# Kernel tuning notes

Measured on AMD Instinct MI355X. Metric: run time of the kernel, lower is better.

## Reference

```python
import jax, jax.numpy as jnp
import numpy as np

EPS = 1e-12  # torch F.normalize clamps the norm at 1e-12

def _l2norm(v, axis):
    n = jnp.sqrt(jnp.sum(v * v, axis=axis, keepdims=True))
    return v / jnp.maximum(n, EPS)

def setup_inputs() -> dict:
    key = jax.random.key(0)
    k1, k2, k3, k4 = jax.random.split(key, 4)
    N, C, H, W, K = 64, 64, 64, 64, 128
    alpha = 1.0
    x = jax.random.normal(k1, (N, C, H, W), dtype=jnp.float32)
    centroids = jax.random.uniform(k2, (K, C), dtype=jnp.float32)
    # conv is initialized from centroids (2*alpha*c, -alpha*||c||) but is an
    # independent parameter after init; keep the init relationship for realism.
    conv_w = 2.0 * alpha * centroids
    conv_b = -alpha * jnp.sqrt(jnp.sum(centroids * centroids, axis=1))
    return {"x": x, "centroids": centroids, "conv_w": conv_w, "conv_b": conv_b}

def reference(x, centroids, conv_w, conv_b):
    N, C, H, W = x.shape
    K = centroids.shape[0]
    # L2-normalize descriptors along channel dim
    xn = _l2norm(x, axis=1)                                   # [N,C,H,W]
    # 1x1 conv == per-pixel linear map C->K
    logits = jnp.einsum('nchw,kc->nkhw', xn, conv_w) + conv_b[None, :, None, None]
    sa = jax.nn.softmax(logits.reshape(N, K, H * W), axis=1)  # [N,K,HW]
    xf = xn.reshape(N, C, H * W)                              # [N,C,HW]
    # vlad[n,k,c] = sum_l sa[n,k,l] * (xf[n,c,l] - centroids[k,c])
    #            = (sa @ xf^T)[n,k,c] - sum_l sa[n,k,l] * centroids[k,c]
    vlad = jnp.einsum('nkl,ncl->nkc', sa, xf) - sa.sum(axis=-1)[:, :, None] * centroids[None]
    vlad = _l2norm(vlad, axis=2)            # intra-normalization per cluster
    vlad = vlad.reshape(N, K * C)
    vlad = _l2norm(vlad, axis=1)            # global L2 normalization
    return vlad
```

## Files before the change

### kernel.cpp

```cpp
#include <hip/hip_runtime.h>
#include <math.h>

#define NIMG   64
#define CDIM   64
#define HWPX   4096
#define KCL    128
#define TL     32
#define SHIFT  10.0f
#define RSQRT128 0.08838834764831845f

#define XP_S 72
#define XC_S 40
#define PH_S 40

typedef __attribute__((ext_vector_type(8))) short short8;
typedef __attribute__((ext_vector_type(4))) float f32x4;

#define MFMA(a, b, c) __builtin_amdgcn_mfma_f32_16x16x32_bf16((a), (b), (c), 0, 0, 0)

#define PERM_HI16 0x07060302u

template <int NP>
__global__ __launch_bounds__(256, 2)
void netvlad_main(const float* __restrict__ x,
                  const float* __restrict__ conv_w,
                  const float* __restrict__ conv_b,
                  float* __restrict__ vout,
                  float* __restrict__ asout,
                  int use_atomic)
{
    constexpr int PIXPART = HWPX / NP;
    constexpr int NCHUNK  = PIXPART / TL;

    __shared__ __align__(16) short xp_hi[TL * XP_S], xp_lo[TL * XP_S];
    __shared__ __align__(16) short xc[CDIM * XC_S];
    __shared__ __align__(16) short ph[KCL * PH_S];
    __shared__ float redA[4 * 33];
    __shared__ float sumP[4 * TL];

    const int t   = threadIdx.x;
    const int w   = t >> 6;
    const int l   = t & 63;
    const int l15 = l & 15, l4 = l >> 4;
    const int n    = blockIdx.x / NP;
    const int part = blockIdx.x - n * NP;
    const int p_s  = t & 31;
    const int sg   = t >> 5;

    short8 wh[2][2], wl[2][2];
    #pragma unroll
    for (int kt = 0; kt < 2; ++kt) {
        const int krow = (2 * w + kt) * 16 + l15;
        #pragma unroll
        for (int ks = 0; ks < 2; ++ks) {
            const float4* wp = (const float4*)(conv_w + krow * CDIM + ks * 32 + l4 * 8);
            float4 wa = wp[0], wb = wp[1];
            float wv[8] = {wa.x, wa.y, wa.z, wa.w, wb.x, wb.y, wb.z, wb.w};
            #pragma unroll
            for (int j = 0; j < 8; ++j) {
                unsigned u = __builtin_bit_cast(unsigned, wv[j]);
                wh[kt][ks][j] = (short)(u >> 16);
                float hf = __builtin_bit_cast(float, u & 0xffff0000u);
                wl[kt][ks][j] = (short)(__builtin_bit_cast(unsigned, wv[j] - hf) >> 16);
            }
        }
    }
    float cbr[2][4];
    #pragma unroll
    for (int kt = 0; kt < 2; ++kt)
        #pragma unroll
        for (int i = 0; i < 4; ++i)
            cbr[kt][i] = conv_b[(2 * w + kt) * 16 + l4 * 4 + i] - SHIFT;

    f32x4 acc2[2][4];
    #pragma unroll
    for (int a = 0; a < 2; ++a)
        #pragma unroll
        for (int b = 0; b < 4; ++b) acc2[a][b] = (f32x4)0.0f;
    float asr[2][4];
    #pragma unroll
    for (int a = 0; a < 2; ++a)
        #pragma unroll
        for (int i = 0; i < 4; ++i) asr[a][i] = 0.f;

    const float* xbase = x + (size_t)n * CDIM * HWPX + part * PIXPART;

    float xv[8];
    #pragma unroll
    for (int j = 0; j < 8; ++j)
        xv[j] = xbase[(sg * 8 + j) * HWPX + p_s];

    for (int ch = 0; ch < NCHUNK; ++ch) {
        float ssq = 0.f;
        #pragma unroll
        for (int j = 0; j < 8; ++j) ssq += xv[j] * xv[j];
        ssq += __shfl_xor(ssq, 32);
        if (l < 32) redA[w * 33 + p_s] = ssq;

        unsigned uh[4], ul[4];
        #pragma unroll
        for (int jp = 0; jp < 4; ++jp) {
            const unsigned u0 = __builtin_bit_cast(unsigned, xv[2 * jp]);
            const unsigned u1 = __builtin_bit_cast(unsigned, xv[2 * jp + 1]);
            uh[jp] = __builtin_amdgcn_perm(u1, u0, PERM_HI16);
            const float h0 = __builtin_bit_cast(float, u0 & 0xffff0000u);
            const float h1 = __builtin_bit_cast(float, u1 & 0xffff0000u);
            const unsigned lo0 = __builtin_bit_cast(unsigned, xv[2 * jp] - h0);
            const unsigned lo1 = __builtin_bit_cast(unsigned, xv[2 * jp + 1] - h1);
            ul[jp] = __builtin_amdgcn_perm(lo1, lo0, PERM_HI16);
        }
        *(uint4*)&xp_hi[p_s * XP_S + sg * 8] = make_uint4(uh[0], uh[1], uh[2], uh[3]);
        *(uint4*)&xp_lo[p_s * XP_S + sg * 8] = make_uint4(ul[0], ul[1], ul[2], ul[3]);

        #pragma unroll
        for (int jp = 0; jp < 4; ++jp) {
            unsigned pk;
            asm("v_cvt_pk_bf16_f32 %0, %1, %2"
                : "=v"(pk) : "v"(xv[2 * jp]), "v"(xv[2 * jp + 1]));
            xc[(sg * 8 + 2 * jp)     * XC_S + p_s] = (short)pk;
            xc[(sg * 8 + 2 * jp + 1) * XC_S + p_s] = (short)(pk >> 16);
        }
        __syncthreads();

        if (ch + 1 < NCHUNK) {
            #pragma unroll
            for (int j = 0; j < 8; ++j)
                xv[j] = xbase[(sg * 8 + j) * HWPX + (ch + 1) * TL + p_s];
        }

        f32x4 a1[2][2];
        #pragma unroll
        for (int a = 0; a < 2; ++a)
            #pragma unroll
            for (int b = 0; b < 2; ++b) a1[a][b] = (f32x4)0.0f;
        #pragma unroll
        for (int ks = 0; ks < 2; ++ks) {
            #pragma unroll
            for (int pt = 0; pt < 2; ++pt) {
                short8 bh = *(short8*)&xp_hi[(pt * 16 + l15) * XP_S + ks * 32 + l4 * 8];
                short8 bl = *(short8*)&xp_lo[(pt * 16 + l15) * XP_S + ks * 32 + l4 * 8];
                #pragma unroll
                for (int kt = 0; kt < 2; ++kt) {
                    a1[kt][pt] = MFMA(wh[kt][ks], bh, a1[kt][pt]);
                    a1[kt][pt] = MFMA(wh[kt][ks], bl, a1[kt][pt]);
                    a1[kt][pt] = MFMA(wl[kt][ks], bh, a1[kt][pt]);
                }
            }
        }

        float rn[2];
        #pragma unroll
        for (int pt = 0; pt < 2; ++pt) {
            const int col = pt * 16 + l15;
            float s0 = redA[col] + redA[33 + col];
            float s1 = redA[2 * 33 + col] + redA[3 * 33 + col];
            rn[pt] = 1.0f / fmaxf(sqrtf(s0 + s1), 1e-12f);
        }

        float e[2][2][4], sp[2] = {0.f, 0.f};
        #pragma unroll
        for (int kt = 0; kt < 2; ++kt)
            #pragma unroll
            for (int pt = 0; pt < 2; ++pt)
                #pragma unroll
                for (int i = 0; i < 4; ++i) {
                    float ev = __expf(fmaf(a1[kt][pt][i], rn[pt], cbr[kt][i]));
                    e[kt][pt][i] = ev;
                    sp[pt] += ev;
                }
        #pragma unroll
        for (int pt = 0; pt < 2; ++pt) {
            sp[pt] += __shfl_xor(sp[pt], 16);
            sp[pt] += __shfl_xor(sp[pt], 32);
        }
        if (l4 == 0) {
            sumP[w * TL + l15]      = sp[0];
            sumP[w * TL + 16 + l15] = sp[1];
        }
        __syncthreads();

        float rden[2], rdn2[2];
        #pragma unroll
        for (int pt = 0; pt < 2; ++pt) {
            const int col = pt * 16 + l15;
            float den = sumP[col] + sumP[TL + col] + sumP[2 * TL + col] + sumP[3 * TL + col];
            rden[pt] = 1.0f / den;
            rdn2[pt] = rden[pt] * rn[pt];
        }

        #pragma unroll
        for (int kt = 0; kt < 2; ++kt)
            #pragma unroll
            for (int i = 0; i < 4; ++i) {
                const int row = (2 * w + kt) * 16 + l4 * 4 + i;
                const float e0 = e[kt][0][i], e1 = e[kt][1][i];
                asr[kt][i] = fmaf(e0, rden[0], asr[kt][i]);
                asr[kt][i] = fmaf(e1, rden[1], asr[kt][i]);
                const float p0 = e0 * rdn2[0], p1 = e1 * rdn2[1];
                unsigned pk;
                asm("v_cvt_pk_bf16_f32 %0, %1, %2" : "=v"(pk) : "v"(p0), "v"(p1));
                ph[row * PH_S + l15]      = (short)pk;
                ph[row * PH_S + 16 + l15] = (short)(pk >> 16);
            }

        {
            short8 xh2[4];
            #pragma unroll
            for (int ct = 0; ct < 4; ++ct)
                xh2[ct] = *(short8*)&xc[(ct * 16 + l15) * XC_S + l4 * 8];
            #pragma unroll
            for (int kt = 0; kt < 2; ++kt) {
                short8 ah = *(short8*)&ph[((2 * w + kt) * 16 + l15) * PH_S + l4 * 8];
                #pragma unroll
                for (int ct = 0; ct < 4; ++ct)
                    acc2[kt][ct] = MFMA(ah, xh2[ct], acc2[kt][ct]);
            }
        }
        __syncthreads();
    }

    float* vg = use_atomic ? vout + (size_t)n * KCL * CDIM
                           : vout + (size_t)blockIdx.x * KCL * CDIM;
    #pragma unroll
    for (int kt = 0; kt < 2; ++kt)
        #pragma unroll
        for (int ct = 0; ct < 4; ++ct)
            #pragma unroll
            for (int i = 0; i < 4; ++i) {
                const int row = (2 * w + kt) * 16 + l4 * 4 + i;
                const int col = ct * 16 + l15;
                if (use_atomic) atomicAdd(&vg[row * CDIM + col], acc2[kt][ct][i]);
                else            vg[row * CDIM + col] = acc2[kt][ct][i];
            }

    #pragma unroll
    for (int kt = 0; kt < 2; ++kt)
        #pragma unroll
        for (int i = 0; i < 4; ++i) {
            float v = asr[kt][i];
            v += __shfl_xor(v, 1); v += __shfl_xor(v, 2);
            v += __shfl_xor(v, 4); v += __shfl_xor(v, 8);
            if (l15 == 0) {
                const int row = (2 * w + kt) * 16 + l4 * 4 + i;
                if (use_atomic) atomicAdd(&asout[n * KCL + row], v);
                else            asout[blockIdx.x * KCL + row] = v;
            }
        }
}

__global__ __launch_bounds__(256)
void netvlad_finalize(const float* __restrict__ vpart,
                      const float* __restrict__ aspart,
                      const float* __restrict__ cent,
                      float* __restrict__ out,
                      int nparts)
{
    const int t = threadIdx.x;
    const int n  = blockIdx.x >> 3;
    const int kg = blockIdx.x & 7;
    const int k  = kg * 16 + (t >> 4);
    const int c0 = (t & 15) * 4;

    float vsum[4] = {0.f, 0.f, 0.f, 0.f};
    float av = 0.f;
    for (int pt = 0; pt < nparts; ++pt) {
        const float* vg = vpart + (((size_t)n * nparts + pt) * KCL + k) * CDIM + c0;
        float4 a = *(const float4*)vg;
        vsum[0] += a.x; vsum[1] += a.y; vsum[2] += a.z; vsum[3] += a.w;
        av += aspart[(n * nparts + pt) * KCL + k];
    }

    float4 cq = *(const float4*)(cent + k * CDIM + c0);
    float cc[4] = {cq.x, cq.y, cq.z, cq.w};
    float ss = 0.f;
    #pragma unroll
    for (int j = 0; j < 4; ++j) {
        vsum[j] -= av * cc[j];
        ss += vsum[j] * vsum[j];
    }
    ss += __shfl_xor(ss, 1); ss += __shfl_xor(ss, 2);
    ss += __shfl_xor(ss, 4); ss += __shfl_xor(ss, 8);
    const float s = (1.0f / fmaxf(sqrtf(ss), 1e-12f)) * RSQRT128;

    float4 o;
    o.x = vsum[0] * s; o.y = vsum[1] * s; o.z = vsum[2] * s; o.w = vsum[3] * s;
    *(float4*)(out + (size_t)n * KCL * CDIM + k * CDIM + c0) = o;
}

extern "C" void kernel_launch(void* const* d_in, const int* in_sizes, int n_in,
                              void* d_out, int out_size, void* d_ws, size_t ws_size,
                              hipStream_t stream) {
    const float* x     = (const float*)d_in[0];
    const float* cent  = (const float*)d_in[1];
    const float* convw = (const float*)d_in[2];
    const float* convb = (const float*)d_in[3];
    float* out = (float*)d_out;

    const size_t need8 = (size_t)NIMG * 8 * (KCL * CDIM + KCL) * sizeof(float);

    if (ws_size >= need8) {
        float* vws  = (float*)d_ws;
        float* asws = vws + (size_t)NIMG * 8 * KCL * CDIM;
        netvlad_main<8><<<dim3(NIMG * 8), dim3(256), 0, stream>>>(
            x, convw, convb, vws, asws, 0);
        netvlad_finalize<<<dim3(NIMG * 8), dim3(256), 0, stream>>>(
            vws, asws, cent, out, 8);
    } else {
        float* vws  = (float*)d_ws;
        float* asws = vws + (size_t)NIMG * KCL * CDIM;
        const size_t zb = (size_t)NIMG * (KCL * CDIM + KCL) * sizeof(float);
        hipMemsetAsync(d_ws, 0, zb, stream);
        netvlad_main<8><<<dim3(NIMG * 8), dim3(256), 0, stream>>>(
            x, convw, convb, vws, asws, 1);
        netvlad_finalize<<<dim3(NIMG * 8), dim3(256), 0, stream>>>(
            vws, asws, cent, out, 1);
    }
}
```

Baseline: 127.3 us.

## Double-buffer LDS pixel staging and prefetch input two chunks ahead

The staged pixel tiles (hi/lo bf16 splits, the bf16 transposed copy, and the per-pixel sum-of-squares) now live in two LDS buffers. The next chunk is converted and written into the alternate buffer at the start of each iteration, before the current chunk's MFMA work. This removes the barrier that used to sit between staging and compute, and moves the global loads two chunks ahead so their latency overlaps more work. The cost is more LDS and longer register live ranges, which could affect occupancy at the 2-blocks-per-CU launch bound.

Result: no change. 124.8 us (-1.9%).

```diff
diff --git a/kernel.cpp b/kernel.cpp
--- a/kernel.cpp
+++ b/kernel.cpp
@@ -32,10 +32,10 @@
     constexpr int PIXPART = HWPX / NP;
     constexpr int NCHUNK  = PIXPART / TL;
 
-    __shared__ __align__(16) short xp_hi[TL * XP_S], xp_lo[TL * XP_S];
-    __shared__ __align__(16) short xc[CDIM * XC_S];
+    __shared__ __align__(16) short xp_hi[2][TL * XP_S], xp_lo[2][TL * XP_S];
+    __shared__ __align__(16) short xc[2][CDIM * XC_S];
     __shared__ __align__(16) short ph[KCL * PH_S];
-    __shared__ float redA[4 * 33];
+    __shared__ float redA[2][4 * 33];
     __shared__ float sumP[4 * TL];
 
     const int t   = threadIdx.x;
@@ -86,16 +86,13 @@
     const float* xbase = x + (size_t)n * CDIM * HWPX + part * PIXPART;
 
     float xv[8];
-    #pragma unroll
-    for (int j = 0; j < 8; ++j)
-        xv[j] = xbase[(sg * 8 + j) * HWPX + p_s];
-
-    for (int ch = 0; ch < NCHUNK; ++ch) {
+
+    auto stage = [&](int buf) {
         float ssq = 0.f;
         #pragma unroll
         for (int j = 0; j < 8; ++j) ssq += xv[j] * xv[j];
         ssq += __shfl_xor(ssq, 32);
-        if (l < 32) redA[w * 33 + p_s] = ssq;
+        if (l < 32) redA[buf][w * 33 + p_s] = ssq;
 
         unsigned uh[4], ul[4];
         #pragma unroll
@@ -109,23 +106,40 @@
             const unsigned lo1 = __builtin_bit_cast(unsigned, xv[2 * jp + 1] - h1);
             ul[jp] = __builtin_amdgcn_perm(lo1, lo0, PERM_HI16);
         }
-        *(uint4*)&xp_hi[p_s * XP_S + sg * 8] = make_uint4(uh[0], uh[1], uh[2], uh[3]);
-        *(uint4*)&xp_lo[p_s * XP_S + sg * 8] = make_uint4(ul[0], ul[1], ul[2], ul[3]);
+        *(uint4*)&xp_hi[buf][p_s * XP_S + sg * 8] = make_uint4(uh[0], uh[1], uh[2], uh[3]);
+        *(uint4*)&xp_lo[buf][p_s * XP_S + sg * 8] = make_uint4(ul[0], ul[1], ul[2], ul[3]);
 
         #pragma unroll
         for (int jp = 0; jp < 4; ++jp) {
             unsigned pk;
             asm("v_cvt_pk_bf16_f32 %0, %1, %2"
                 : "=v"(pk) : "v"(xv[2 * jp]), "v"(xv[2 * jp + 1]));
-            xc[(sg * 8 + 2 * jp)     * XC_S + p_s] = (short)pk;
-            xc[(sg * 8 + 2 * jp + 1) * XC_S + p_s] = (short)(pk >> 16);
-        }
-        __syncthreads();
+            xc[buf][(sg * 8 + 2 * jp)     * XC_S + p_s] = (short)pk;
+            xc[buf][(sg * 8 + 2 * jp + 1) * XC_S + p_s] = (short)(pk >> 16);
+        }
+    };
+
+    #pragma unroll
+    for (int j = 0; j < 8; ++j)
+        xv[j] = xbase[(sg * 8 + j) * HWPX + p_s];
+    stage(0);
+    if (NCHUNK > 1) {
+        #pragma unroll
+        for (int j = 0; j < 8; ++j)
+            xv[j] = xbase[(sg * 8 + j) * HWPX + TL + p_s];
+    }
+    __syncthreads();
+
+    for (int ch = 0; ch < NCHUNK; ++ch) {
+        const int cur = ch & 1;
 
         if (ch + 1 < NCHUNK) {
-            #pragma unroll
-            for (int j = 0; j < 8; ++j)
-                xv[j] = xbase[(sg * 8 + j) * HWPX + (ch + 1) * TL + p_s];
+            stage(cur ^ 1);
+            if (ch + 2 < NCHUNK) {
+                #pragma unroll
+                for (int j = 0; j < 8; ++j)
+                    xv[j] = xbase[(sg * 8 + j) * HWPX + (ch + 2) * TL + p_s];
+            }
         }
 
         f32x4 a1[2][2];
@@ -137,8 +151,8 @@
         for (int ks = 0; ks < 2; ++ks) {
             #pragma unroll
             for (int pt = 0; pt < 2; ++pt) {
-                short8 bh = *(short8*)&xp_hi[(pt * 16 + l15) * XP_S + ks * 32 + l4 * 8];
-                short8 bl = *(short8*)&xp_lo[(pt * 16 + l15) * XP_S + ks * 32 + l4 * 8];
+                short8 bh = *(short8*)&xp_hi[cur][(pt * 16 + l15) * XP_S + ks * 32 + l4 * 8];
+                short8 bl = *(short8*)&xp_lo[cur][(pt * 16 + l15) * XP_S + ks * 32 + l4 * 8];
                 #pragma unroll
                 for (int kt = 0; kt < 2; ++kt) {
                     a1[kt][pt] = MFMA(wh[kt][ks], bh, a1[kt][pt]);
@@ -152,8 +166,8 @@
         #pragma unroll
         for (int pt = 0; pt < 2; ++pt) {
             const int col = pt * 16 + l15;
-            float s0 = redA[col] + redA[33 + col];
-            float s1 = redA[2 * 33 + col] + redA[3 * 33 + col];
+            float s0 = redA[cur][col] + redA[cur][33 + col];
+            float s1 = redA[cur][2 * 33 + col] + redA[cur][3 * 33 + col];
             rn[pt] = 1.0f / fmaxf(sqrtf(s0 + s1), 1e-12f);
         }
 
@@ -207,7 +221,7 @@
             short8 xh2[4];
             #pragma unroll
             for (int ct = 0; ct < 4; ++ct)
-                xh2[ct] = *(short8*)&xc[(ct * 16 + l15) * XC_S + l4 * 8];
+                xh2[ct] = *(short8*)&xc[cur][(ct * 16 + l15) * XC_S + l4 * 8];
             #pragma unroll
             for (int kt = 0; kt < 2; ++kt) {
                 short8 ah = *(short8*)&ph[((2 * w + kt) * 16 + l15) * PH_S + l4 * 8];
```
